# Performance work log

Hardware: AMD Instinct MI355X
Metric: run time of the kernel (lower is better)

Reference implementation:

```python
import jax, jax.numpy as jnp
import numpy as np

TEMPERATURE = 0.5
EPS = 1e-12  # torch F.normalize eps


def _l2_normalize(x, axis):
    norm = jnp.sqrt(jnp.sum(x * x, axis=axis, keepdims=True))
    return x / jnp.maximum(norm, EPS)


def setup_inputs() -> dict:
    key = jax.random.key(0)
    k1, k2 = jax.random.split(key)
    B, C, H, W = 16, 256, 64, 64
    teacher_vectors = jax.random.normal(k1, (B, C, H, W), dtype=jnp.float32)
    student_vectors = jax.random.normal(k2, (B, C, H, W), dtype=jnp.float32)
    return {"teacher_vectors": teacher_vectors, "student_vectors": student_vectors}


def reference(teacher_vectors, student_vectors):
    B, C, H, W = teacher_vectors.shape
    T = TEMPERATURE
    # first normalize over class dim (dim=1), as in the torch module
    t = _l2_normalize(teacher_vectors, axis=1)
    s = _l2_normalize(student_vectors, axis=1)
    # per-sample: view (C, H*W) and row-normalize
    t = _l2_normalize(t.reshape(B, C, H * W), axis=2)  # [B, C, D]
    s = _l2_normalize(s.reshape(B, C, H * W), axis=2)  # [B, C, D]
    # batched similarity: student @ teacher^T per sample -> [B, C, C]
    sim = jnp.einsum('bcd,bed->bce', s, t)
    pos = jnp.diagonal(sim, axis1=1, axis2=2)  # [B, C]
    # -log(exp(pos/T) / sum(exp(sim/T))) = -pos/T + logsumexp(sim/T)
    lse = jax.nn.logsumexp(sim.reshape(B, C * C) / T, axis=1)  # [B]
    per_sample = jnp.mean(-pos / T + lse[:, None], axis=1)  # mean over classes
    return jnp.mean(per_sample)
```

## Files before the change

### kernel.cpp

```cpp
#include <hip/hip_runtime.h>
#include <hip/hip_bf16.h>

typedef short bf16x8 __attribute__((ext_vector_type(8)));
typedef float f32x4 __attribute__((ext_vector_type(4)));

#define GLOAD(gp, lp)                                                          \
    __builtin_amdgcn_global_load_lds(                                          \
        (const __attribute__((address_space(1))) void*)(gp),                   \
        (__attribute__((address_space(3))) void*)(lp), 16, 0, 0)

static constexpr int kB = 16;
static constexpr int kC = 256;
static constexpr int kHW = 4096;

static constexpr int OFF_INVC_T = 0;
static constexpr int OFF_INVC_S = 65536;
static constexpr int OFF_INVD_T = 131072;
static constexpr int OFF_INVD_S = 135168;
static constexpr int OFF_EXPS   = 139264;
static constexpr int OFF_POSS   = 139280;
static constexpr size_t OFF_U_BYTES = 139296ull * 4ull;
static constexpr size_t U_ELEMS = (size_t)kB * kC * kHW;
static constexpr size_t OFF_PSIM = 139296ull + 16777216ull;

__global__ void colnorm_k(const float* __restrict__ ten,
                          const float* __restrict__ stu,
                          float* __restrict__ ws)
{
    int tid = threadIdx.x;
    if (blockIdx.x == 0 && blockIdx.y == 0 && tid < 32)
        ws[OFF_EXPS + tid] = 0.0f;

    const float* src = (blockIdx.y == 0) ? ten : stu;
    float* invC = ws + ((blockIdx.y == 0) ? OFF_INVC_T : OFF_INVC_S);

    int g  = blockIdx.x * 256 + tid;
    int b  = g >> 12;
    int hw = g & 4095;
    const float* p = src + (size_t)b * (kC * kHW) + hw;

    float a0 = 0.0f, a1 = 0.0f;
#pragma unroll 8
    for (int c = 0; c < kC; c += 2) {
        float v0 = p[(size_t)c * kHW];
        float v1 = p[(size_t)(c + 1) * kHW];
        a0 += v0 * v0;
        a1 += v1 * v1;
    }
    invC[g] = 1.0f / fmaxf(sqrtf(a0 + a1), 1e-12f);
}

__device__ __forceinline__ unsigned short f2bf(float f) {
    __hip_bfloat16 h = __float2bfloat16(f);
    return __builtin_bit_cast(unsigned short, h);
}

__global__ void rownorm_k(const float* __restrict__ ten,
                          const float* __restrict__ stu,
                          float* __restrict__ ws)
{
    int tid = threadIdx.x;
    int bc  = blockIdx.x;
    int b   = bc >> 8;
    bool isT = (blockIdx.y == 0);
    const float* src  = isT ? ten : stu;
    const float* invC = ws + (isT ? OFF_INVC_T : OFF_INVC_S);
    float* invD       = ws + (isT ? OFF_INVD_T : OFF_INVD_S);
    unsigned short* u = (unsigned short*)((char*)ws + OFF_U_BYTES) + (isT ? 0 : U_ELEMS);

    size_t rowBase = (size_t)bc * kHW;
    const float* crow = invC + b * kHW;

    float ss = 0.0f;
#pragma unroll
    for (int it = 0; it < 4; ++it) {
        int off = it * 1024 + tid * 4;
        float4 v = *(const float4*)(src + rowBase + off);
        float4 s = *(const float4*)(crow + off);
        float u0 = v.x * s.x, u1 = v.y * s.y, u2 = v.z * s.z, u3 = v.w * s.w;
        ss += u0 * u0 + u1 * u1 + u2 * u2 + u3 * u3;
        ushort4 o;
        o.x = f2bf(u0); o.y = f2bf(u1); o.z = f2bf(u2); o.w = f2bf(u3);
        *(ushort4*)(u + rowBase + off) = o;
    }
#pragma unroll
    for (int o = 32; o; o >>= 1) ss += __shfl_down(ss, o);
    __shared__ float red[4];
    if ((tid & 63) == 0) red[tid >> 6] = ss;
    __syncthreads();
    if (tid == 0)
        invD[bc] = 1.0f / fmaxf(sqrtf(red[0] + red[1] + red[2] + red[3]), 1e-12f);
}

__global__ __launch_bounds__(256) void gemm_part_k(float* __restrict__ ws,
                                                   int kIters)
{
    const unsigned short* uT = (const unsigned short*)((const char*)ws + OFF_U_BYTES);
    const unsigned short* uS = uT + U_ELEMS;
    float* psim = ws + OFF_PSIM;

    __shared__ __align__(16) unsigned short As[2][4096];
    __shared__ __align__(16) unsigned short Bs[2][4096];

    int tid = threadIdx.x;
    int bid = blockIdx.x;
    int cpx = gridDim.x >> 3;
    int w   = (bid & 7) * cpx + (bid >> 3);
    int tile = w & 15;
    int g    = w >> 4;
    int b    = g & 15;
    int kz   = g >> 4;
    int tr   = tile >> 2, tc = tile & 3;
    int lane = tid & 63, wid = tid >> 6;
    int wr   = wid >> 1, wc = wid & 1;

    int k0base = kz * (kIters * 64);

    int D0  = tid * 16;
    int r0s = D0 >> 7;
    int c0s = ((D0 & 127) ^ ((r0s & 7) << 4)) >> 1;
    int D1  = 4096 + tid * 16;
    int r1s = D1 >> 7;
    int c1s = ((D1 & 127) ^ ((r1s & 7) << 4)) >> 1;

    const unsigned short* gA = uS + ((size_t)(b * kC + tr * 64) << 12) + k0base;
    const unsigned short* gB = uT + ((size_t)(b * kC + tc * 64) << 12) + k0base;

    f32x4 acc[2][2] = {};

    GLOAD(gA + ((size_t)r0s << 12) + c0s, (char*)As[0] + D0);
    GLOAD(gA + ((size_t)r1s << 12) + c1s, (char*)As[0] + D1);
    GLOAD(gB + ((size_t)r0s << 12) + c0s, (char*)Bs[0] + D0);
    GLOAD(gB + ((size_t)r1s << 12) + c1s, (char*)Bs[0] + D1);
    __syncthreads();

    int cur = 0;
    for (int it = 0; it < kIters; ++it) {
        if (it + 1 < kIters) {
            int k0 = (it + 1) * 64;
            GLOAD(gA + ((size_t)r0s << 12) + k0 + c0s, (char*)As[cur ^ 1] + D0);
            GLOAD(gA + ((size_t)r1s << 12) + k0 + c1s, (char*)As[cur ^ 1] + D1);
            GLOAD(gB + ((size_t)r0s << 12) + k0 + c0s, (char*)Bs[cur ^ 1] + D0);
            GLOAD(gB + ((size_t)r1s << 12) + k0 + c1s, (char*)Bs[cur ^ 1] + D1);
        }
        const char* Ab = (const char*)As[cur];
        const char* Bb = (const char*)Bs[cur];
#pragma unroll
        for (int ks = 0; ks < 2; ++ks) {
            bf16x8 av[2], bv[2];
            int kb = ks * 64 + (lane >> 4) * 16;
#pragma unroll
            for (int f = 0; f < 2; ++f) {
                int row = wr * 32 + f * 16 + (lane & 15);
                av[f] = *(const bf16x8*)(Ab + (row << 7) + (kb ^ ((row & 7) << 4)));
                int col = wc * 32 + f * 16 + (lane & 15);
                bv[f] = *(const bf16x8*)(Bb + (col << 7) + (kb ^ ((col & 7) << 4)));
            }
#pragma unroll
            for (int fr = 0; fr < 2; ++fr)
#pragma unroll
                for (int fc = 0; fc < 2; ++fc)
                    acc[fr][fc] = __builtin_amdgcn_mfma_f32_16x16x32_bf16(
                        av[fr], bv[fc], acc[fr][fc], 0, 0, 0);
        }
        __syncthreads();
        cur ^= 1;
    }

    float* pt = psim + ((size_t)(kz * 16 + b) << 16);
#pragma unroll
    for (int fr = 0; fr < 2; ++fr)
#pragma unroll
        for (int fc = 0; fc < 2; ++fc) {
            int col = tc * 64 + wc * 32 + fc * 16 + (lane & 15);
#pragma unroll
            for (int j = 0; j < 4; ++j) {
                int row = tr * 64 + wr * 32 + fr * 16 + (lane >> 4) * 4 + j;
                pt[row * 256 + col] = acc[fr][fc][j];
            }
        }
}

__global__ __launch_bounds__(256) void reduce_k(float* __restrict__ ws, int KS)
{
    const float* psim  = ws + OFF_PSIM;
    const float* invDt = ws + OFF_INVD_T;
    const float* invDs = ws + OFF_INVD_S;

    int b     = blockIdx.x >> 6;
    int local = ((blockIdx.x & 63) << 10) + threadIdx.x * 4;
    int row   = local >> 8;
    int col   = local & 255;

    float4 s = {0.0f, 0.0f, 0.0f, 0.0f};
    for (int ks = 0; ks < KS; ++ks) {
        float4 v = *(const float4*)(psim + (((size_t)(ks * 16 + b)) << 16) + local);
        s.x += v.x; s.y += v.y; s.z += v.z; s.w += v.w;
    }
    float  ds = invDs[b * 256 + row];
    float4 dt = *(const float4*)(invDt + b * 256 + col);
    float v0 = s.x * ds * dt.x;
    float v1 = s.y * ds * dt.y;
    float v2 = s.z * ds * dt.z;
    float v3 = s.w * ds * dt.w;

    float eAcc = __expf(2.0f * v0) + __expf(2.0f * v1) +
                 __expf(2.0f * v2) + __expf(2.0f * v3);
    float pAcc = 0.0f;
    if (row == col)     pAcc = v0;
    if (row == col + 1) pAcc = v1;
    if (row == col + 2) pAcc = v2;
    if (row == col + 3) pAcc = v3;

#pragma unroll
    for (int o = 32; o; o >>= 1) {
        eAcc += __shfl_down(eAcc, o);
        pAcc += __shfl_down(pAcc, o);
    }
    __shared__ float redE[4], redP[4];
    int lane = threadIdx.x & 63, wid = threadIdx.x >> 6;
    if (lane == 0) { redE[wid] = eAcc; redP[wid] = pAcc; }
    __syncthreads();
    if (threadIdx.x == 0) {
        atomicAdd(ws + OFF_EXPS + b, redE[0] + redE[1] + redE[2] + redE[3]);
        atomicAdd(ws + OFF_POSS + b, redP[0] + redP[1] + redP[2] + redP[3]);
    }
}

__global__ void finalize_k(const float* __restrict__ ws, float* __restrict__ out)
{
    if (threadIdx.x == 0) {
        const float* expSum = ws + OFF_EXPS;
        const float* posSum = ws + OFF_POSS;
        float loss = 0.0f;
        for (int b = 0; b < kB; ++b)
            loss += -2.0f * posSum[b] / (float)kC + logf(expSum[b]);
        out[0] = loss / (float)kB;
    }
}

extern "C" void kernel_launch(void* const* d_in, const int* in_sizes, int n_in,
                              void* d_out, int out_size, void* d_ws, size_t ws_size,
                              hipStream_t stream)
{
    const float* ten = (const float*)d_in[0];
    const float* stu = (const float*)d_in[1];
    float* ws  = (float*)d_ws;
    float* out = (float*)d_out;

    int KS = 4;
    {
        size_t base = OFF_PSIM * 4ull;
        if (ws_size < base + 4ull * 16 * 65536 * 4) KS = 2;
        if (ws_size < base + 2ull * 16 * 65536 * 4) KS = 1;
    }
    int kIters = (kHW / KS) / 64;

    colnorm_k<<<dim3(256, 2), 256, 0, stream>>>(ten, stu, ws);
    rownorm_k<<<dim3(4096, 2), 256, 0, stream>>>(ten, stu, ws);
    gemm_part_k<<<dim3(256 * KS), 256, 0, stream>>>(ws, kIters);
    reduce_k<<<dim3(1024), 256, 0, stream>>>(ws, KS);
    finalize_k<<<1, 64, 0, stream>>>(ws, out);
}
```

Before: 110.4 us.

## Split channel-norm reduction across channel slices with vectorized loads and finalize pass

The column-norm kernel used only 512 blocks, each walking all 256 channels with scalar loads. It now launches 1024 blocks that each sum squares over a 32-channel slice with float4 loads, writing partial sums into the PSIM workspace region. A small follow-up kernel adds the 8 partials and computes the inverse norms. This is meant to raise memory-level parallelism on the 128 MB input read, at the cost of an extra launch and a partial-sum round trip through workspace.

```diff
diff --git a/kernel.cpp b/kernel.cpp
--- a/kernel.cpp
+++ b/kernel.cpp
@@ -23,31 +23,55 @@
 static constexpr size_t U_ELEMS = (size_t)kB * kC * kHW;
 static constexpr size_t OFF_PSIM = 139296ull + 16777216ull;
 
-__global__ void colnorm_k(const float* __restrict__ ten,
-                          const float* __restrict__ stu,
-                          float* __restrict__ ws)
+__global__ __launch_bounds__(256) void colnorm_part_k(const float* __restrict__ ten,
+                                                      const float* __restrict__ stu,
+                                                      float* __restrict__ ws)
 {
     int tid = threadIdx.x;
-    if (blockIdx.x == 0 && blockIdx.y == 0 && tid < 32)
-        ws[OFF_EXPS + tid] = 0.0f;
-
-    const float* src = (blockIdx.y == 0) ? ten : stu;
-    float* invC = ws + ((blockIdx.y == 0) ? OFF_INVC_T : OFF_INVC_S);
-
-    int g  = blockIdx.x * 256 + tid;
-    int b  = g >> 12;
-    int hw = g & 4095;
-    const float* p = src + (size_t)b * (kC * kHW) + hw;
-
-    float a0 = 0.0f, a1 = 0.0f;
+    int t   = blockIdx.x;
+    if (t == 0 && tid < 32) ws[OFF_EXPS + tid] = 0.0f;
+
+    int hwc = t & 3;
+    int cs  = (t >> 2) & 7;
+    int b   = (t >> 5) & 15;
+    int ts  = t >> 9;
+    const float* src = ts ? stu : ten;
+
+    int hw0 = hwc * 1024 + tid * 4;
+    const float* p = src + (size_t)b * (kC * kHW) + (size_t)cs * 32 * kHW + hw0;
+
+    float4 acc = {0.0f, 0.0f, 0.0f, 0.0f};
 #pragma unroll 8
-    for (int c = 0; c < kC; c += 2) {
-        float v0 = p[(size_t)c * kHW];
-        float v1 = p[(size_t)(c + 1) * kHW];
-        a0 += v0 * v0;
-        a1 += v1 * v1;
-    }
-    invC[g] = 1.0f / fmaxf(sqrtf(a0 + a1), 1e-12f);
+    for (int c = 0; c < 32; ++c) {
+        float4 v = *(const float4*)(p + (size_t)c * kHW);
+        acc.x += v.x * v.x;
+        acc.y += v.y * v.y;
+        acc.z += v.z * v.z;
+        acc.w += v.w * v.w;
+    }
+    float* part = ws + OFF_PSIM + ((size_t)(ts * 8 + cs) << 16) + b * kHW + hw0;
+    *(float4*)part = acc;
+}
+
+__global__ __launch_bounds__(256) void invc_fin_k(float* __restrict__ ws)
+{
+    int g0  = (blockIdx.x * 256 + threadIdx.x) * 4;
+    int ts  = g0 >> 16;
+    int pos = g0 & 65535;
+
+    const float* part = ws + OFF_PSIM + ((size_t)(ts * 8) << 16) + pos;
+    float4 s = {0.0f, 0.0f, 0.0f, 0.0f};
+#pragma unroll
+    for (int cs = 0; cs < 8; ++cs) {
+        float4 v = *(const float4*)(part + ((size_t)cs << 16));
+        s.x += v.x; s.y += v.y; s.z += v.z; s.w += v.w;
+    }
+    float4 o;
+    o.x = 1.0f / fmaxf(sqrtf(s.x), 1e-12f);
+    o.y = 1.0f / fmaxf(sqrtf(s.y), 1e-12f);
+    o.z = 1.0f / fmaxf(sqrtf(s.z), 1e-12f);
+    o.w = 1.0f / fmaxf(sqrtf(s.w), 1e-12f);
+    *(float4*)(ws + (ts ? OFF_INVC_S : OFF_INVC_T) + pos) = o;
 }
 
 __device__ __forceinline__ unsigned short f2bf(float f) {
@@ -256,7 +280,8 @@
     }
     int kIters = (kHW / KS) / 64;
 
-    colnorm_k<<<dim3(256, 2), 256, 0, stream>>>(ten, stu, ws);
+    colnorm_part_k<<<dim3(1024), 256, 0, stream>>>(ten, stu, ws);
+    invc_fin_k<<<dim3(128), 256, 0, stream>>>(ws);
     rownorm_k<<<dim3(4096, 2), 256, 0, stream>>>(ten, stu, ws);
     gemm_part_k<<<dim3(256 * KS), 256, 0, stream>>>(ws, kIters);
     reduce_k<<<dim3(1024), 256, 0, stream>>>(ws, KS);
```

New measurement: 94.15 us. 1.17x faster.
